# Kernel tuning notes

Measured on AMD Instinct MI355X. Metric: run time of the kernel, lower is better.

## Reference

```python
import jax, jax.numpy as jnp
import numpy as np

L, D, H, DFF, A, S = 8, 1024, 16, 4096, 4096, 66
T = S + 1  # 67 after pool token
DK = D // H
EPS = 1e-5


def _pos_enc(t, d):
    pos = np.arange(t, dtype=np.float32)[:, None]
    div = np.exp(np.arange(0, d, 2, dtype=np.float32) * (-np.log(10000.0) / d))
    pe = np.zeros((t, d), dtype=np.float32)
    pe[:, 0::2] = np.sin(pos * div)
    pe[:, 1::2] = np.cos(pos * div)
    return jnp.asarray(pe)


def _ln(x, g, b):
    m = jnp.mean(x, axis=-1, keepdims=True)
    v = jnp.mean(jnp.square(x - m), axis=-1, keepdims=True)
    return (x - m) * jax.lax.rsqrt(v + EPS) * g + b


def setup_inputs() -> dict:
    key = jax.random.key(0)
    ks = jax.random.split(key, 12)
    B = 256
    sc = 0.02
    return {
        "x": jax.random.randint(ks[0], (B, S), 0, A, dtype=jnp.int32),
        "emb": jax.random.normal(ks[1], (A, D), jnp.float32) * sc,
        "pool": jax.random.normal(ks[2], (D,), jnp.float32) * sc,
        "Wq": jax.random.normal(ks[3], (L, D, D), jnp.float32) * sc,
        "Wk": jax.random.normal(ks[4], (L, D, D), jnp.float32) * sc,
        "Wv": jax.random.normal(ks[5], (L, D, D), jnp.float32) * sc,
        "Wo": jax.random.normal(ks[6], (L, D, D), jnp.float32) * sc,
        "rel_bias": jax.random.normal(ks[7], (L, H, 78, 78), jnp.float32) * sc,
        "ln1_g": jnp.ones((L, D), jnp.float32),
        "ln1_b": jnp.zeros((L, D), jnp.float32),
        "ln2_g": jnp.ones((L, D), jnp.float32),
        "ln2_b": jnp.zeros((L, D), jnp.float32),
        "W1": jax.random.normal(ks[8], (L, D, DFF), jnp.float32) * sc,
        "b1": jnp.zeros((L, DFF), jnp.float32),
        "W2": jax.random.normal(ks[9], (L, DFF, D), jnp.float32) * sc,
        "b2": jnp.zeros((L, D), jnp.float32),
        "Wout": jax.random.normal(ks[10], (D, A), jnp.float32) * sc,
        "bout": jnp.zeros((A,), jnp.float32),
    }


def reference(x, emb, pool, Wq, Wk, Wv, Wo, rel_bias, ln1_g, ln1_b, ln2_g, ln2_b,
              W1, b1, W2, b2, Wout, bout):
    B = x.shape[0]
    h = emb[x] * jnp.sqrt(jnp.float32(D))            # (B, S, D)
    h = jnp.concatenate([jnp.broadcast_to(pool, (B, 1, D)), h], axis=1)  # (B, T, D)
    h = h + _pos_enc(T, D)[None]
    scale = 1.0 / jnp.sqrt(jnp.float32(DK))
    for i in range(L):
        q = (h @ Wq[i]).reshape(B, T, H, DK)
        k = (h @ Wk[i]).reshape(B, T, H, DK)
        v = (h @ Wv[i]).reshape(B, T, H, DK)
        scores = jnp.einsum("bqhd,bkhd->bhqk", q, k) * scale + rel_bias[i][:, :T, :T]
        attn = jax.nn.softmax(scores, axis=-1)
        ctx = jnp.einsum("bhqk,bkhd->bqhd", attn, v).reshape(B, T, D)
        h = _ln(h + ctx @ Wo[i], ln1_g[i], ln1_b[i])
        f = jax.nn.gelu(h @ W1[i] + b1[i], approximate=False) @ W2[i] + b2[i]
        h = _ln(h + f, ln2_g[i], ln2_b[i])
    return h[:, 0, :] @ Wout + bout  # (B, A)
```

## Files before the change

kernel.cpp:

```cpp
#include <hip/hip_runtime.h>
#include <math.h>

typedef unsigned short u16;
typedef __attribute__((ext_vector_type(8))) short short8;
typedef __attribute__((ext_vector_type(4))) float f32x4;

#define LAYERS 8
#define D 1024
#define NH 16
#define DKH 64
#define DFF 4096
#define SEQ 66
#define TT 67
#define BATCH 256
#define ROWS (BATCH*TT)
#define VOCAB 4096
#define TP 80
#define KP 96
#define QS 3072

__device__ __forceinline__ float bf2f(u16 v){
  unsigned int u = ((unsigned int)v) << 16;
  return __builtin_bit_cast(float, u);
}
__device__ __forceinline__ u16 f2bf(float f){
  unsigned int u = __builtin_bit_cast(unsigned int, f);
  u += 0x7FFFu + ((u >> 16) & 1u);
  return (u16)(u >> 16);
}
__device__ __forceinline__ void gload16(const u16* g, u16* l){
  __builtin_amdgcn_global_load_lds((const __attribute__((address_space(1))) void*)g,
                                   (__attribute__((address_space(3))) void*)l, 16, 0, 0);
}

__device__ __forceinline__ void tc_tile(const float* __restrict__ src, u16* __restrict__ dst,
                                        int R, int C, int bx, int by, int tx, int ty){
  __shared__ float tile[32][33];
  const int c0 = bx * 32, r0 = by * 32;
  #pragma unroll
  for (int i = 0; i < 32; i += 8)
    tile[ty + i][tx] = src[(size_t)(r0 + ty + i) * C + (c0 + tx)];
  __syncthreads();
  #pragma unroll
  for (int i = 0; i < 32; i += 8)
    dst[(size_t)(c0 + ty + i) * R + (r0 + tx)] = f2bf(tile[tx][ty + i]);
}

__global__ void transpose6(const float* __restrict__ Wq, const float* __restrict__ Wk,
                           const float* __restrict__ Wv, const float* __restrict__ Wo,
                           const float* __restrict__ W1, const float* __restrict__ W2,
                           u16* __restrict__ WqkvT, u16* __restrict__ WoT,
                           u16* __restrict__ W1T, u16* __restrict__ W2T){
  const int tx = threadIdx.x, ty = threadIdx.y;
  int b = blockIdx.x;
  if (b < 4096){
    const int which = b >> 10, idx = b & 1023;
    const float* s = which == 0 ? Wq : which == 1 ? Wk : which == 2 ? Wv : Wo;
    u16* d = which == 3 ? WoT : WqkvT + which * D * D;
    tc_tile(s, d, D, D, idx & 31, idx >> 5, tx, ty);
  } else if (b < 8192){
    const int idx = b - 4096;
    tc_tile(W1, W1T, D, DFF, idx & 127, idx >> 7, tx, ty);
  } else {
    const int idx = b - 8192;
    tc_tile(W2, W2T, DFF, D, idx & 31, idx >> 5, tx, ty);
  }
}

__global__ void transpose_cast(const float* __restrict__ src, u16* __restrict__ dst,
                               int R, int C){
  tc_tile(src, dst, R, C, blockIdx.x, blockIdx.y, threadIdx.x, threadIdx.y);
}

__global__ void embed_kernel(const int* __restrict__ x, const float* __restrict__ emb,
                             const float* __restrict__ pool, float* __restrict__ h,
                             u16* __restrict__ hb){
  const int row = blockIdx.x;
  const int b = row / TT, t = row % TT;
  const int d0 = threadIdx.x * 4;
  float v[4];
  if (t == 0){
    const float4 p4 = *(const float4*)&pool[d0];
    v[0] = p4.x; v[1] = p4.y; v[2] = p4.z; v[3] = p4.w;
  } else {
    const int id = x[b * SEQ + (t - 1)];
    const float4 e4 = *(const float4*)&emb[(size_t)id * D + d0];
    v[0] = e4.x * 32.f; v[1] = e4.y * 32.f; v[2] = e4.z * 32.f; v[3] = e4.w * 32.f;
  }
  const float c = -logf(10000.f) / (float)D;
  float o[4];
  #pragma unroll
  for (int j = 0; j < 4; j++){
    const int d = d0 + j;
    const int p = d >> 1;
    const float freq = expf((float)(2 * p) * c);
    const float ang = (float)t * freq;
    const float pe = (d & 1) ? cosf(ang) : sinf(ang);
    o[j] = v[j] + pe;
  }
  *(float4*)&h[(size_t)row * D + d0] = make_float4(o[0], o[1], o[2], o[3]);
  const unsigned int lo = (unsigned)f2bf(o[0]) | ((unsigned)f2bf(o[1]) << 16);
  const unsigned int hi = (unsigned)f2bf(o[2]) | ((unsigned)f2bf(o[3]) << 16);
  *(uint2*)&hb[(size_t)row * D + d0] = make_uint2(lo, hi);
}

__global__ void ln_kernel(float* __restrict__ h, const u16* __restrict__ res,
                          u16* __restrict__ hb, const float* __restrict__ g,
                          const float* __restrict__ bta){
  const int row = blockIdx.x;
  const int tid = threadIdx.x;
  const size_t off = (size_t)row * D + tid * 4;
  const float4 a = *(const float4*)&h[off];
  const uint2 r2 = *(const uint2*)&res[off];
  const float s0 = a.x + bf2f((u16)(r2.x & 0xffff));
  const float s1 = a.y + bf2f((u16)(r2.x >> 16));
  const float s2 = a.z + bf2f((u16)(r2.y & 0xffff));
  const float s3 = a.w + bf2f((u16)(r2.y >> 16));
  float sum = s0 + s1 + s2 + s3;
  float sq = s0*s0 + s1*s1 + s2*s2 + s3*s3;
  #pragma unroll
  for (int m = 32; m >= 1; m >>= 1){ sum += __shfl_xor(sum, m); sq += __shfl_xor(sq, m); }
  __shared__ float red[2][4];
  const int w = tid >> 6;
  if ((tid & 63) == 0){ red[0][w] = sum; red[1][w] = sq; }
  __syncthreads();
  sum = red[0][0] + red[0][1] + red[0][2] + red[0][3];
  sq  = red[1][0] + red[1][1] + red[1][2] + red[1][3];
  const float mean = sum * (1.f / D);
  const float var = sq * (1.f / D) - mean * mean;
  const float rs = rsqrtf(var + 1e-5f);
  const float4 gv = *(const float4*)&g[tid * 4];
  const float4 bv = *(const float4*)&bta[tid * 4];
  const float o0 = (s0 - mean) * rs * gv.x + bv.x;
  const float o1 = (s1 - mean) * rs * gv.y + bv.y;
  const float o2 = (s2 - mean) * rs * gv.z + bv.z;
  const float o3 = (s3 - mean) * rs * gv.w + bv.w;
  *(float4*)&h[off] = make_float4(o0, o1, o2, o3);
  const unsigned int lo = (unsigned)f2bf(o0) | ((unsigned)f2bf(o1) << 16);
  const unsigned int hi = (unsigned)f2bf(o2) | ((unsigned)f2bf(o3) << 16);
  *(uint2*)&hb[off] = make_uint2(lo, hi);
}

__global__ __launch_bounds__(256) void attn_kernel(const u16* __restrict__ qkv,
    const float* __restrict__ rel, u16* __restrict__ ctxb){
  __shared__ u16 Qf[8 * 81 * 8];
  __shared__ u16 Kf[8 * 81 * 8];
  __shared__ u16 Vf[12 * 65 * 8];
  __shared__ u16 Pf[12 * 81 * 8];
  __shared__ float Ss[TP][84];
  const int bh = blockIdx.x;
  const int b = bh >> 4, hh = bh & 15;
  const int tid = threadIdx.x, w = tid >> 6, l = tid & 63;
  const size_t qvbase = (size_t)(b * TT) * QS + hh * DKH;
  const size_t obase  = (size_t)(b * TT) * D + hh * DKH;

  {
    const int r0 = tid >> 4, c4 = (tid & 15) * 4;
    const int g = c4 >> 3, e = c4 & 7;
    for (int r = r0; r < TP; r += 16){
      uint2 q2 = make_uint2(0u, 0u), k2 = make_uint2(0u, 0u);
      if (r < TT){
        q2 = *(const uint2*)&qkv[qvbase + (size_t)r * QS + c4];
        k2 = *(const uint2*)&qkv[qvbase + 1024 + (size_t)r * QS + c4];
      }
      *(uint2*)&Qf[(g * 81 + r) * 8 + e] = q2;
      *(uint2*)&Kf[(g * 81 + r) * 8 + e] = k2;
    }
    for (int j = r0; j < KP; j += 16){
      u16 v4[4] = {0, 0, 0, 0};
      if (j < TT) *(uint2*)v4 = *(const uint2*)&qkv[qvbase + 2048 + (size_t)j * QS + c4];
      const int gg = j >> 3, ee = j & 7;
      #pragma unroll
      for (int d = 0; d < 4; d++)
        Vf[(gg * 65 + (c4 + d)) * 8 + ee] = v4[d];
    }
  }
  __syncthreads();

  const int fr = l & 15, gg = l >> 4;
  for (int p = w; p < 25; p += 4){
    const int rt = p / 5, ct = p % 5;
    f32x4 acc = {};
    #pragma unroll
    for (int kk = 0; kk < 2; kk++){
      const short8 a  = *(const short8*)&Qf[((kk * 4 + gg) * 81 + rt * 16 + fr) * 8];
      const short8 bf = *(const short8*)&Kf[((kk * 4 + gg) * 81 + ct * 16 + fr) * 8];
      acc = __builtin_amdgcn_mfma_f32_16x16x32_bf16(a, bf, acc, 0, 0, 0);
    }
    const int col = ct * 16 + fr;
    #pragma unroll
    for (int r = 0; r < 4; r++){
      const int row = rt * 16 + gg * 4 + r;
      float sv = -1e30f;
      if (row < TT && col < TT)
        sv = acc[r] * 0.125f + rel[((size_t)hh * 78 + row) * 78 + col];
      Ss[row][col] = sv;
    }
  }
  __syncthreads();

  for (int row = w; row < TP; row += 4){
    const float s1 = Ss[row][l];
    const float s2 = (l < 16) ? Ss[row][64 + l] : -1e30f;
    float mx = fmaxf(s1, s2);
    #pragma unroll
    for (int m = 32; m >= 1; m >>= 1) mx = fmaxf(mx, __shfl_xor(mx, m));
    const float e1 = __expf(s1 - mx);
    const float e2 = (l < 16) ? __expf(s2 - mx) : 0.f;
    float sum = e1 + e2;
    #pragma unroll
    for (int m = 32; m >= 1; m >>= 1) sum += __shfl_xor(sum, m);
    const float inv = 1.f / sum;
    Pf[((l >> 3) * 81 + row) * 8 + (l & 7)] = f2bf(e1 * inv);
    if (l < 16){
      Pf[((8  + (l >> 3)) * 81 + row) * 8 + (l & 7)] = f2bf(e2 * inv);
      Pf[((10 + (l >> 3)) * 81 + row) * 8 + (l & 7)] = 0;
    }
  }
  __syncthreads();

  for (int p = w; p < 20; p += 4){
    const int rt = p >> 2, ct = p & 3;
    f32x4 acc = {};
    #pragma unroll
    for (int kk = 0; kk < 3; kk++){
      const short8 a  = *(const short8*)&Pf[((kk * 4 + gg) * 81 + rt * 16 + fr) * 8];
      const short8 bf = *(const short8*)&Vf[((kk * 4 + gg) * 65 + ct * 16 + fr) * 8];
      acc = __builtin_amdgcn_mfma_f32_16x16x32_bf16(a, bf, acc, 0, 0, 0);
    }
    #pragma unroll
    for (int r = 0; r < 4; r++){
      const int row = rt * 16 + gg * 4 + r;
      if (row < TT)
        ctxb[obase + (size_t)row * D + ct * 16 + fr] = f2bf(acc[r]);
    }
  }
}

template<int OBF16, int BIAS, int GELU>
__global__ __launch_bounds__(256, 2) void gemm_bt(
    const u16* __restrict__ A, int lda,
    const u16* __restrict__ Bt,
    void* __restrict__ Cv, int ldc,
    const float* __restrict__ bias, int K, int nby)
{
  __shared__ u16 As[2][128 * 32];
  __shared__ u16 Bs[2][128 * 32];
  const int nwg = gridDim.x, bid = blockIdx.x;
  const int q8 = nwg >> 3, r8 = nwg & 7;
  const int xcd = bid & 7, off = bid >> 3;
  const int wg = (xcd < r8 ? xcd * (q8 + 1) : r8 * (q8 + 1) + (xcd - r8) * q8) + off;
  const int m0 = (wg / nby) * 128, n0 = (wg % nby) * 128;

  const int tid = threadIdx.x;
  const int l = tid & 63, w = tid >> 6;
  const int wr = w >> 1, wc = w & 1;
  f32x4 acc[4][4] = {};
  const int lr = l >> 2;
  const int lseg = (l & 3) * 8;
  const u16* ga0 = A + (size_t)(m0 + w * 32 + lr) * lda + lseg;
  const u16* ga1 = A + (size_t)(m0 + w * 32 + 16 + lr) * lda + lseg;
  const u16* gb0 = Bt + (size_t)(n0 + w * 32 + lr) * K + lseg;
  const u16* gb1 = Bt + (size_t)(n0 + w * 32 + 16 + lr) * K + lseg;
  const int fr = l & 15, kg = (l >> 4) * 8;

#define STAGE(sel, kc) do { \
    gload16(ga0 + (kc), &As[sel][(w * 32) * 32]); \
    gload16(ga1 + (kc), &As[sel][(w * 32 + 16) * 32]); \
    gload16(gb0 + (kc), &Bs[sel][(w * 32) * 32]); \
    gload16(gb1 + (kc), &Bs[sel][(w * 32 + 16) * 32]); \
  } while (0)

  const int nkt = K >> 5;
  STAGE(0, 0);
  __syncthreads();
  int cur = 0;
  #pragma unroll 1
  for (int kt = 0; kt < nkt; ++kt){
    if (kt + 1 < nkt) STAGE(cur ^ 1, (kt + 1) * 32);
    short8 af[4], bf[4];
    #pragma unroll
    for (int i = 0; i < 4; i++){
      af[i] = *(const short8*)&As[cur][(wr * 64 + i * 16 + fr) * 32 + kg];
      bf[i] = *(const short8*)&Bs[cur][(wc * 64 + i * 16 + fr) * 32 + kg];
    }
    #pragma unroll
    for (int i = 0; i < 4; i++)
      #pragma unroll
      for (int j = 0; j < 4; j++)
        acc[i][j] = __builtin_amdgcn_mfma_f32_16x16x32_bf16(af[i], bf[j], acc[i][j], 0, 0, 0);
    __syncthreads();
    cur ^= 1;
  }
#undef STAGE

  const int rg = (l >> 4) * 4;
  #pragma unroll
  for (int i = 0; i < 4; i++){
    #pragma unroll
    for (int j = 0; j < 4; j++){
      const int col = n0 + wc * 64 + j * 16 + fr;
      const float bv = BIAS ? bias[col] : 0.f;
      #pragma unroll
      for (int r = 0; r < 4; r++){
        const int row = m0 + wr * 64 + i * 16 + rg + r;
        float xv = acc[i][j][r] + bv;
        if (GELU) xv = 0.5f * xv * (1.f + erff(xv * 0.70710678118f));
        if (OBF16) ((u16*)Cv)[(size_t)row * ldc + col] = f2bf(xv);
        else       ((float*)Cv)[(size_t)row * ldc + col] = xv;
      }
    }
  }
}

extern "C" void kernel_launch(void* const* d_in, const int* in_sizes, int n_in,
                              void* d_out, int out_size, void* d_ws, size_t ws_size,
                              hipStream_t stream) {
  const int*   x       = (const int*)  d_in[0];
  const float* emb     = (const float*)d_in[1];
  const float* pool    = (const float*)d_in[2];
  const float* Wq      = (const float*)d_in[3];
  const float* Wk      = (const float*)d_in[4];
  const float* Wv      = (const float*)d_in[5];
  const float* Wo      = (const float*)d_in[6];
  const float* rel     = (const float*)d_in[7];
  const float* ln1_g   = (const float*)d_in[8];
  const float* ln1_b   = (const float*)d_in[9];
  const float* ln2_g   = (const float*)d_in[10];
  const float* ln2_b   = (const float*)d_in[11];
  const float* W1      = (const float*)d_in[12];
  const float* b1      = (const float*)d_in[13];
  const float* W2      = (const float*)d_in[14];
  const float* b2      = (const float*)d_in[15];
  const float* Wout    = (const float*)d_in[16];
  const float* bout    = (const float*)d_in[17];
  float* out = (float*)d_out;

  const size_t SZ_WDD  = (size_t)D * D * 2;
  const size_t SZ_WDF  = (size_t)D * DFF * 2;
  const size_t SZ_H    = (size_t)ROWS * D * 4;
  const size_t SZ_HB   = (size_t)ROWS * D * 2;
  const size_t need = 4*SZ_WDD + 3*SZ_WDF + SZ_H + 6*SZ_HB;
  if (ws_size < need) return;

  char* p = (char*)d_ws;
  u16* WqkvT = (u16*)p; p += 3*SZ_WDD;
  u16* WoT   = (u16*)p; p += SZ_WDD;
  u16* W1T   = (u16*)p; p += SZ_WDF;
  u16* W2T   = (u16*)p; p += SZ_WDF;
  u16* WouT  = (u16*)p; p += SZ_WDF;
  float* h   = (float*)p; p += SZ_H;
  u16* hb    = (u16*)p; p += SZ_HB;
  u16* qkv   = (u16*)p; p += 3*SZ_HB;
  u16* ctxb  = (u16*)p; p += SZ_HB;
  u16* gb    = qkv;
  u16* tmpb  = (u16*)p; p += SZ_HB;

  dim3 tb(32, 8);
  transpose_cast<<<dim3(VOCAB/32, D/32), tb, 0, stream>>>(Wout, WouT, D, VOCAB);
  embed_kernel<<<ROWS, 256, 0, stream>>>(x, emb, pool, h, hb);

  const int MB = ROWS / 128;
  for (int l = 0; l < LAYERS; ++l){
    const size_t wo = (size_t)l * D * D;
    const size_t wf = (size_t)l * D * DFF;
    transpose6<<<12288, tb, 0, stream>>>(Wq + wo, Wk + wo, Wv + wo, Wo + wo,
                                         W1 + wf, W2 + wf, WqkvT, WoT, W1T, W2T);

    gemm_bt<1,0,0><<<MB * (QS/128),  256, 0, stream>>>(hb, D, WqkvT, qkv, QS, nullptr, D, QS/128);
    attn_kernel<<<BATCH*NH, 256, 0, stream>>>(qkv, rel + (size_t)l*NH*78*78, ctxb);
    gemm_bt<1,0,0><<<MB * (D/128),   256, 0, stream>>>(ctxb, D, WoT, tmpb, D, nullptr, D, D/128);
    ln_kernel<<<ROWS, 256, 0, stream>>>(h, tmpb, hb, ln1_g + l*D, ln1_b + l*D);
    gemm_bt<1,1,1><<<MB * (DFF/128), 256, 0, stream>>>(hb, D, W1T, gb, DFF, b1 + l*DFF, D, DFF/128);
    gemm_bt<1,1,0><<<MB * (D/128),   256, 0, stream>>>(gb, DFF, W2T, tmpb, D, b2 + l*D, DFF, D/128);
    ln_kernel<<<ROWS, 256, 0, stream>>>(h, tmpb, hb, ln2_g + l*D, ln2_b + l*D);
  }
  gemm_bt<0,1,0><<<(BATCH/128) * (VOCAB/128), 256, 0, stream>>>(
      hb, TT * D, WouT, out, VOCAB, bout, D, VOCAB/128);
}
```

Measured before the change: 6.656 ms.

## Drop fp32 residual stream, raise GEMM occupancy bound, use nontemporal stores

Removes the fp32 hidden-state buffer and keeps the residual stream only in bf16, so embed and layernorm read and write half the bytes. The layernorm now works in place on the bf16 buffer. The GEMM launch bound changes from 2 to 4 waves per SIMD, which can force register spills with the 4x4 accumulator tile. GEMM output stores become nontemporal. Keeping the residual in bf16 loses precision across the 8 layers.

New measurement: 6.870 ms. 1.03x slower.

```diff
diff --git a/kernel.cpp b/kernel.cpp
--- a/kernel.cpp
+++ b/kernel.cpp
@@ -73,8 +73,7 @@
 }
 
 __global__ void embed_kernel(const int* __restrict__ x, const float* __restrict__ emb,
-                             const float* __restrict__ pool, float* __restrict__ h,
-                             u16* __restrict__ hb){
+                             const float* __restrict__ pool, u16* __restrict__ hb){
   const int row = blockIdx.x;
   const int b = row / TT, t = row % TT;
   const int d0 = threadIdx.x * 4;
@@ -98,24 +97,22 @@
     const float pe = (d & 1) ? cosf(ang) : sinf(ang);
     o[j] = v[j] + pe;
   }
-  *(float4*)&h[(size_t)row * D + d0] = make_float4(o[0], o[1], o[2], o[3]);
   const unsigned int lo = (unsigned)f2bf(o[0]) | ((unsigned)f2bf(o[1]) << 16);
   const unsigned int hi = (unsigned)f2bf(o[2]) | ((unsigned)f2bf(o[3]) << 16);
   *(uint2*)&hb[(size_t)row * D + d0] = make_uint2(lo, hi);
 }
 
-__global__ void ln_kernel(float* __restrict__ h, const u16* __restrict__ res,
-                          u16* __restrict__ hb, const float* __restrict__ g,
-                          const float* __restrict__ bta){
+__global__ void ln_kernel(u16* __restrict__ hio, const u16* __restrict__ res,
+                          const float* __restrict__ g, const float* __restrict__ bta){
   const int row = blockIdx.x;
   const int tid = threadIdx.x;
   const size_t off = (size_t)row * D + tid * 4;
-  const float4 a = *(const float4*)&h[off];
+  const uint2 a2 = *(const uint2*)&hio[off];
   const uint2 r2 = *(const uint2*)&res[off];
-  const float s0 = a.x + bf2f((u16)(r2.x & 0xffff));
-  const float s1 = a.y + bf2f((u16)(r2.x >> 16));
-  const float s2 = a.z + bf2f((u16)(r2.y & 0xffff));
-  const float s3 = a.w + bf2f((u16)(r2.y >> 16));
+  const float s0 = bf2f((u16)(a2.x & 0xffff)) + bf2f((u16)(r2.x & 0xffff));
+  const float s1 = bf2f((u16)(a2.x >> 16))    + bf2f((u16)(r2.x >> 16));
+  const float s2 = bf2f((u16)(a2.y & 0xffff)) + bf2f((u16)(r2.y & 0xffff));
+  const float s3 = bf2f((u16)(a2.y >> 16))    + bf2f((u16)(r2.y >> 16));
   float sum = s0 + s1 + s2 + s3;
   float sq = s0*s0 + s1*s1 + s2*s2 + s3*s3;
   #pragma unroll
@@ -135,10 +132,9 @@
   const float o1 = (s1 - mean) * rs * gv.y + bv.y;
   const float o2 = (s2 - mean) * rs * gv.z + bv.z;
   const float o3 = (s3 - mean) * rs * gv.w + bv.w;
-  *(float4*)&h[off] = make_float4(o0, o1, o2, o3);
   const unsigned int lo = (unsigned)f2bf(o0) | ((unsigned)f2bf(o1) << 16);
   const unsigned int hi = (unsigned)f2bf(o2) | ((unsigned)f2bf(o3) << 16);
-  *(uint2*)&hb[off] = make_uint2(lo, hi);
+  *(uint2*)&hio[off] = make_uint2(lo, hi);
 }
 
 __global__ __launch_bounds__(256) void attn_kernel(const u16* __restrict__ qkv,
@@ -238,7 +234,7 @@
 }
 
 template<int OBF16, int BIAS, int GELU>
-__global__ __launch_bounds__(256, 2) void gemm_bt(
+__global__ __launch_bounds__(256, 4) void gemm_bt(
     const u16* __restrict__ A, int lda,
     const u16* __restrict__ Bt,
     void* __restrict__ Cv, int ldc,
@@ -306,8 +302,8 @@
         const int row = m0 + wr * 64 + i * 16 + rg + r;
         float xv = acc[i][j][r] + bv;
         if (GELU) xv = 0.5f * xv * (1.f + erff(xv * 0.70710678118f));
-        if (OBF16) ((u16*)Cv)[(size_t)row * ldc + col] = f2bf(xv);
-        else       ((float*)Cv)[(size_t)row * ldc + col] = xv;
+        if (OBF16) __builtin_nontemporal_store(f2bf(xv), &((u16*)Cv)[(size_t)row * ldc + col]);
+        else       __builtin_nontemporal_store(xv, &((float*)Cv)[(size_t)row * ldc + col]);
       }
     }
   }
@@ -338,9 +334,8 @@
 
   const size_t SZ_WDD  = (size_t)D * D * 2;
   const size_t SZ_WDF  = (size_t)D * DFF * 2;
-  const size_t SZ_H    = (size_t)ROWS * D * 4;
   const size_t SZ_HB   = (size_t)ROWS * D * 2;
-  const size_t need = 4*SZ_WDD + 3*SZ_WDF + SZ_H + 6*SZ_HB;
+  const size_t need = 4*SZ_WDD + 3*SZ_WDF + 6*SZ_HB;
   if (ws_size < need) return;
 
   char* p = (char*)d_ws;
@@ -349,7 +344,6 @@
   u16* W1T   = (u16*)p; p += SZ_WDF;
   u16* W2T   = (u16*)p; p += SZ_WDF;
   u16* WouT  = (u16*)p; p += SZ_WDF;
-  float* h   = (float*)p; p += SZ_H;
   u16* hb    = (u16*)p; p += SZ_HB;
   u16* qkv   = (u16*)p; p += 3*SZ_HB;
   u16* ctxb  = (u16*)p; p += SZ_HB;
@@ -358,7 +352,7 @@
 
   dim3 tb(32, 8);
   transpose_cast<<<dim3(VOCAB/32, D/32), tb, 0, stream>>>(Wout, WouT, D, VOCAB);
-  embed_kernel<<<ROWS, 256, 0, stream>>>(x, emb, pool, h, hb);
+  embed_kernel<<<ROWS, 256, 0, stream>>>(x, emb, pool, hb);
 
   const int MB = ROWS / 128;
   for (int l = 0; l < LAYERS; ++l){
@@ -370,10 +364,10 @@
     gemm_bt<1,0,0><<<MB * (QS/128),  256, 0, stream>>>(hb, D, WqkvT, qkv, QS, nullptr, D, QS/128);
     attn_kernel<<<BATCH*NH, 256, 0, stream>>>(qkv, rel + (size_t)l*NH*78*78, ctxb);
     gemm_bt<1,0,0><<<MB * (D/128),   256, 0, stream>>>(ctxb, D, WoT, tmpb, D, nullptr, D, D/128);
-    ln_kernel<<<ROWS, 256, 0, stream>>>(h, tmpb, hb, ln1_g + l*D, ln1_b + l*D);
+    ln_kernel<<<ROWS, 256, 0, stream>>>(hb, tmpb, ln1_g + l*D, ln1_b + l*D);
     gemm_bt<1,1,1><<<MB * (DFF/128), 256, 0, stream>>>(hb, D, W1T, gb, DFF, b1 + l*DFF, D, DFF/128);
     gemm_bt<1,1,0><<<MB * (D/128),   256, 0, stream>>>(gb, DFF, W2T, tmpb, D, b2 + l*D, DFF, D/128);
-    ln_kernel<<<ROWS, 256, 0, stream>>>(h, tmpb, hb, ln2_g + l*D, ln2_b + l*D);
+    ln_kernel<<<ROWS, 256, 0, stream>>>(hb, tmpb, ln2_g + l*D, ln2_b + l*D);
   }
   gemm_bt<0,1,0><<<(BATCH/128) * (VOCAB/128), 256, 0, stream>>>(
       hb, TT * D, WouT, out, VOCAB, bout, D, VOCAB/128);
```
